# Kernel optimization log

Measured on AMD Instinct MI355X. Metric: run time of the kernel, lower is better.

## Reference

```python
import jax, jax.numpy as jnp
import numpy as np
from jax import lax

# --- hyperparameters from init_kwargs ---
THRESH = 0.5
TAU_M = 20.0
DT = 1.0
LENS = 0.5
GRAD_MAX = 1.0
DECAY = float(np.exp(-DT / TAU_M))  # leaky membrane decay (exp LUT approximated exactly)


@jax.custom_vjp
def spike_fn(v):
    # hard threshold spike
    return (v > THRESH).astype(v.dtype)


def _spike_fwd(v):
    return spike_fn(v), v


def _spike_bwd(v, g):
    # rectangular surrogate gradient (LUT-quantized in original; analytic here),
    # clipped at grad_max
    surr = jnp.minimum((jnp.abs(v - THRESH) < LENS).astype(g.dtype) / (2.0 * LENS), GRAD_MAX)
    return (g * surr,)


spike_fn.defvjp(_spike_fwd, _spike_bwd)


def conv2d(x, w):
    # NCHW, OIHW, stride 1, pad 1 (same)
    return lax.conv_general_dilated(x, w, (1, 1), [(1, 1), (1, 1)],
                                    dimension_numbers=('NCHW', 'OIHW', 'NCHW'))


def maxpool2(x):
    return lax.reduce_window(x, -jnp.inf, lax.max, (1, 1, 2, 2), (1, 1, 2, 2), 'VALID')


def lif_update(vm, s_prev, I):
    # leaky integrate with reset-by-subtraction via (1 - spike) gating
    vm = vm * DECAY * (1.0 - s_prev) + I
    return vm, spike_fn(vm)


def _xavier(key, shape, fan_in, fan_out):
    a = np.sqrt(6.0 / (fan_in + fan_out))
    return jax.random.uniform(key, shape, jnp.float32, -a, a)


def setup_inputs() -> dict:
    key = jax.random.key(0)
    k0, k1, k2, k3, k4 = jax.random.split(key, 5)
    B, T, C, H, W = 16, 16, 2, 64, 64
    inp = jax.random.uniform(k0, (B, T, C, H, W), jnp.float32)
    W0 = _xavier(k1, (32, 2, 3, 3), 2 * 9, 32 * 9)
    W1 = _xavier(k2, (64, 32, 3, 3), 32 * 9, 64 * 9)
    D0 = _xavier(k3, (512, 65536), 65536, 512)
    D1 = _xavier(k4, (11, 512), 512, 11)
    return {"input": inp, "W0": W0, "W1": W1, "D0": D0, "D1": D1,
            "batch_size": 16, "num_steps": 16, "limit": 1}


def reference(input, W0, W1, D0, D1, batch_size, num_steps, limit):
    B = batch_size
    vm0 = jnp.zeros((B, 32, 64, 64), jnp.float32); s0 = jnp.zeros_like(vm0)
    vm1 = jnp.zeros((B, 64, 64, 64), jnp.float32); s1 = jnp.zeros_like(vm1)
    vm2 = jnp.zeros((B, 512), jnp.float32); s2 = jnp.zeros_like(vm2)
    vm3 = jnp.zeros((B, 11), jnp.float32); s3 = jnp.zeros_like(vm3)
    acc = jnp.zeros((B, 11), jnp.float32)

    xs = jnp.swapaxes(input, 0, 1)  # [T, B, C, H, W] time-major for scan

    def step(carry, x_t):
        vm0, s0, vm1, s1, vm2, s2, vm3, s3, acc = carry
        in_spike = jnp.clip(x_t, 0.0, 1.0) if limit else x_t
        # conv layer 0 (no pool after layer 0 per original control flow)
        vm0, s0 = lif_update(vm0, s0, conv2d(in_spike, W0))
        # conv layer 1 (last conv): pool then flatten
        vm1, s1 = lif_update(vm1, s1, conv2d(s0, W1))
        flat = maxpool2(s1).reshape(s1.shape[0], -1)  # [B, 64*32*32]
        # dense layers
        vm2, s2 = lif_update(vm2, s2, flat @ D0.T)
        vm3, s3 = lif_update(vm3, s3, s2 @ D1.T)
        acc = acc + s3
        return (vm0, s0, vm1, s1, vm2, s2, vm3, s3, acc), None

    carry = (vm0, s0, vm1, s1, vm2, s2, vm3, s3, acc)
    carry, _ = lax.scan(step, carry, xs[:num_steps])
    return carry[-1] / num_steps
```

## Files before the change

### kernel.cpp

```cpp
#include <hip/hip_runtime.h>
#include <hip/hip_bf16.h>
#include <stdint.h>

#define DECAY 0.951229424500714f

#define BATCH 16
#define TSTEPS 16

#define OFF_S0BITS 0u
#define OFF_W0TB 4460544u
#define OFF_W1TB 4462848u
#define ZERO_BYTES 4460544u
#define KSPLIT 64
#define KCHUNK (65536 / KSPLIT)
#define OFF_PART_BYTES 0u
#define OFF_I_BYTES 33554432u
#define OFF_FLAT_BYTES 34078720u

typedef __attribute__((ext_vector_type(8))) short short8;
typedef __attribute__((ext_vector_type(4))) float floatx4;

__device__ inline unsigned short f2bf_rne(float f) {
    unsigned u = __float_as_uint(f);
    unsigned r = (u + 0x7FFFu + ((u >> 16) & 1u)) >> 16;
    return (unsigned short)r;
}
__device__ inline float bf2f(unsigned short h) {
    return __uint_as_float(((unsigned)h) << 16);
}

__global__ __launch_bounds__(256) void prep_weights(const float* __restrict__ W0,
                                                    const float* __restrict__ W1,
                                                    float* __restrict__ ws) {
    int id = blockIdx.x * 256 + threadIdx.x;
    if (id < 18432) {
        int oh = id / 9216, rem = id % 9216;
        int ic = rem / 288, rem2 = rem % 288;
        int k = rem2 / 32, ocl = rem2 % 32;
        int oc = oh * 32 + ocl;
        float* w1t = (float*)((char*)ws + OFF_W1TB);
        w1t[id] = W1[((size_t)oc * 32 + ic) * 9 + k];
    } else if (id < 19008) {
        int e = id - 18432;
        int ict = e >> 5, oc = e & 31;
        int ic = ict / 9, tap = ict % 9;
        float* w0t = (float*)((char*)ws + OFF_W0TB);
        w0t[ict * 32 + oc] = W0[(oc * 2 + ic) * 9 + tap];
    }
}

__global__ __launch_bounds__(256) void conv0_all(const float* __restrict__ in,
                                                 float* __restrict__ ws) {
    int b = blockIdx.x, y = blockIdx.y;
    int tid = threadIdx.x;
    int x = tid & 63;
    int g = __builtin_amdgcn_readfirstlane(tid >> 6);
    const float* w0t = (const float*)((const char*)ws + OFF_W0TB);
    unsigned char* s0b = (unsigned char*)((char*)ws + OFF_S0BITS);

    float vm[8];
#pragma unroll
    for (int u = 0; u < 8; ++u) vm[u] = 0.f;

    for (int t = 0; t < TSTEPS; ++t) {
        const float* xin = in + (size_t)((b * TSTEPS + t) * 2) * 4096;
        float acc[8];
#pragma unroll
        for (int u = 0; u < 8; ++u) acc[u] = 0.f;
#pragma unroll
        for (int ic = 0; ic < 2; ++ic) {
#pragma unroll
            for (int dy = 0; dy < 3; ++dy) {
                int sy = y + dy - 1;
                bool vy = (unsigned)sy < 64u;
                const float* rp = xin + ic * 4096 + sy * 64;
#pragma unroll
                for (int dx = 0; dx < 3; ++dx) {
                    int sx = x + dx - 1;
                    float v = (vy && (unsigned)sx < 64u) ? rp[sx] : 0.f;
                    v = fminf(fmaxf(v, 0.f), 1.f);
                    const float* wp = w0t + ((ic * 9 + dy * 3 + dx) * 32 + g * 8);
#pragma unroll
                    for (int u = 0; u < 8; ++u) acc[u] = fmaf(v, wp[u], acc[u]);
                }
            }
        }
        unsigned byte = 0;
#pragma unroll
        for (int u = 0; u < 8; ++u) {
            float v = ((vm[u] > 0.5f) ? 0.f : vm[u] * DECAY) + acc[u];
            vm[u] = v;
            if (v > 0.5f) byte |= (1u << u);
        }
        s0b[((size_t)(t * 16 + b) * 4356 + (size_t)(y + 1) * 66 + (x + 1)) * 4 + g] =
            (unsigned char)byte;
    }
}

__global__ __launch_bounds__(256, 4) void conv1_all(float* __restrict__ ws) {
    __shared__ float wlds[32 * 9 * 32];
    int tid = threadIdx.x;
    int j = tid & 31;
    int o4 = tid >> 5;
    int b = blockIdx.x, y2 = blockIdx.y, oh = blockIdx.z;
    int y0 = y2 * 2;

    {
        const float* wsrc = (const float*)((const char*)ws + OFF_W1TB) + (size_t)oh * 9216;
#pragma unroll
        for (int i = 0; i < 9; ++i) {
            int e = tid + i * 256;
            *(float4*)&wlds[e * 4] = *(const float4*)&wsrc[e * 4];
        }
    }
    __syncthreads();

    const unsigned* s0w = (const unsigned*)((const char*)ws + OFF_S0BITS);
    unsigned short* flat2 = (unsigned short*)((char*)ws + OFF_FLAT_BYTES);

    float vm1r[4][2][2];
#pragma unroll
    for (int u = 0; u < 4; ++u)
#pragma unroll
        for (int r = 0; r < 2; ++r)
#pragma unroll
            for (int c = 0; c < 2; ++c) vm1r[u][r][c] = 0.f;

    for (int t = 0; t < TSTEPS; ++t) {
        unsigned bits[4][4];
        {
            const unsigned* p = s0w + (size_t)(t * 16 + b) * 4356 + (size_t)y0 * 66 + 2 * j;
#pragma unroll
            for (int rr = 0; rr < 4; ++rr)
#pragma unroll
                for (int cc = 0; cc < 4; ++cc)
                    bits[rr][cc] = p[rr * 66 + cc];
        }
        unsigned orall = 0;
#pragma unroll
        for (int rr = 0; rr < 4; ++rr)
#pragma unroll
            for (int cc = 0; cc < 4; ++cc) orall |= bits[rr][cc];

        float acc[4][2][2];
#pragma unroll
        for (int u = 0; u < 4; ++u)
#pragma unroll
            for (int r = 0; r < 2; ++r)
#pragma unroll
                for (int c = 0; c < 2; ++c) acc[u][r][c] = 0.f;

        for (int ic = 0; ic < 32; ++ic) {
            if (__ballot((orall >> ic) & 1u) == 0ull) continue;
            float va[4][4];
#pragma unroll
            for (int rr = 0; rr < 4; ++rr)
#pragma unroll
                for (int cc = 0; cc < 4; ++cc)
                    va[rr][cc] = (float)((bits[rr][cc] >> ic) & 1u);
            const float* wic = &wlds[ic * 288 + o4 * 4];
#pragma unroll
            for (int k = 0; k < 9; ++k) {
                int kr = k / 3, kc = k - kr * 3;
                float4 wv = *(const float4*)&wic[k * 32];
                float wk[4] = {wv.x, wv.y, wv.z, wv.w};
#pragma unroll
                for (int u = 0; u < 4; ++u) {
                    float w = wk[u];
#pragma unroll
                    for (int r = 0; r < 2; ++r)
#pragma unroll
                        for (int c = 0; c < 2; ++c)
                            acc[u][r][c] = fmaf(va[kr + r][kc + c], w, acc[u][r][c]);
                }
            }
        }

        int m = t * 16 + b;
#pragma unroll
        for (int u = 0; u < 4; ++u) {
            int oc = oh * 32 + o4 * 4 + u;
            unsigned short por = 0;
#pragma unroll
            for (int r = 0; r < 2; ++r)
#pragma unroll
                for (int c = 0; c < 2; ++c) {
                    float v = vm1r[u][r][c];
                    v = ((v > 0.5f) ? 0.f : v * DECAY) + acc[u][r][c];
                    vm1r[u][r][c] = v;
                    if (v > 0.5f) por = 0x3F80;
                }
            int kg = oc * 128 + y2 * 4 + (j >> 3);
            flat2[((size_t)kg * 256 + m) * 8 + (j & 7)] = por;
        }
    }
}

__global__ __launch_bounds__(256) void dense0_mfma(const float* __restrict__ D0,
                                                   float* __restrict__ ws) {
    __shared__ unsigned short Bh_s[32 * 72];
    __shared__ unsigned short Bl_s[32 * 72];
    int tid = threadIdx.x;
    int kc = blockIdx.x, nb = blockIdx.y;
    int lane = tid & 63, w = tid >> 6, q = lane >> 4, r = lane & 15;
    const unsigned short* flat2 = (const unsigned short*)((const char*)ws + OFF_FLAT_BYTES);

    floatx4 acc[4][2];
#pragma unroll
    for (int i = 0; i < 4; ++i)
#pragma unroll
        for (int jj = 0; jj < 2; ++jj) acc[i][jj] = (floatx4){0.f, 0.f, 0.f, 0.f};

    int bn = tid & 31, bk8 = tid >> 5;
    const float* bG = D0 + (size_t)(nb * 32 + bn) * 65536 + (size_t)kc * KCHUNK + bk8 * 8;

    for (int k0 = 0; k0 < KCHUNK; k0 += 64) {
        short8 af[2][4];
#pragma unroll
        for (int ksi = 0; ksi < 2; ++ksi) {
            int kg = kc * 128 + (k0 >> 3) + ksi * 4 + q;
#pragma unroll
            for (int mi = 0; mi < 4; ++mi)
                af[ksi][mi] = *(const short8*)&flat2[((size_t)kg * 256
                                                     + (w * 64 + mi * 16 + r)) * 8];
        }
        float4 bv0 = *(const float4*)(bG + k0);
        float4 bv1 = *(const float4*)(bG + k0 + 4);

        __syncthreads();
        {
            float f[8] = {bv0.x, bv0.y, bv0.z, bv0.w, bv1.x, bv1.y, bv1.z, bv1.w};
            unsigned hw[4], lw[4];
#pragma unroll
            for (int jj = 0; jj < 4; ++jj) {
                unsigned short h0 = f2bf_rne(f[2*jj]),   h1 = f2bf_rne(f[2*jj+1]);
                unsigned short l0 = f2bf_rne(f[2*jj]   - bf2f(h0));
                unsigned short l1 = f2bf_rne(f[2*jj+1] - bf2f(h1));
                hw[jj] = (unsigned)h0 | ((unsigned)h1 << 16);
                lw[jj] = (unsigned)l0 | ((unsigned)l1 << 16);
            }
            *(uint4*)&Bh_s[bn * 72 + bk8 * 8] = make_uint4(hw[0], hw[1], hw[2], hw[3]);
            *(uint4*)&Bl_s[bn * 72 + bk8 * 8] = make_uint4(lw[0], lw[1], lw[2], lw[3]);
        }
        __syncthreads();

#pragma unroll
        for (int ksi = 0; ksi < 2; ++ksi) {
#pragma unroll
            for (int ni = 0; ni < 2; ++ni) {
                short8 bh = *(const short8*)&Bh_s[(ni * 16 + r) * 72 + ksi * 32 + q * 8];
                short8 bl = *(const short8*)&Bl_s[(ni * 16 + r) * 72 + ksi * 32 + q * 8];
#pragma unroll
                for (int mi = 0; mi < 4; ++mi) {
                    acc[mi][ni] = __builtin_amdgcn_mfma_f32_16x16x32_bf16(af[ksi][mi], bh, acc[mi][ni], 0, 0, 0);
                    acc[mi][ni] = __builtin_amdgcn_mfma_f32_16x16x32_bf16(af[ksi][mi], bl, acc[mi][ni], 0, 0, 0);
                }
            }
        }
    }

    float* part = (float*)((char*)ws + OFF_PART_BYTES);
#pragma unroll
    for (int mi = 0; mi < 4; ++mi)
#pragma unroll
        for (int ni = 0; ni < 2; ++ni) {
            int m0 = w * 64 + mi * 16 + q * 4;
            int n  = nb * 32 + ni * 16 + r;
#pragma unroll
            for (int rg = 0; rg < 4; ++rg)
                part[((size_t)kc * 256 + m0 + rg) * 512 + n] = acc[mi][ni][rg];
        }
}

__global__ __launch_bounds__(256) void reduce_part(float* __restrict__ ws) {
    int e = blockIdx.x * 256 + threadIdx.x;
    const float* part = (const float*)((const char*)ws + OFF_PART_BYTES);
    float s = 0.f;
#pragma unroll 8
    for (int c = 0; c < KSPLIT; ++c) s += part[(size_t)c * 131072 + e];
    ((float*)((char*)ws + OFF_I_BYTES))[e] = s;
}

__global__ __launch_bounds__(512) void tail_kernel(const float* __restrict__ D1,
                                                   float* __restrict__ out,
                                                   const float* __restrict__ ws_ro) {
    __shared__ float s2l[512];
    __shared__ float d1l[11 * 512];
    __shared__ float pb[2][11];
    int b = blockIdx.x;
    int tid = threadIdx.x;
    for (int i = tid; i < 11 * 512; i += 512) d1l[i] = D1[i];
    const float* Ibuf = (const float*)((const char*)ws_ro + OFF_I_BYTES);

    float vm2 = 0.f;
    unsigned s2 = 0u;
    float vm3 = 0.f, s3 = 0.f, accv = 0.f;
    __syncthreads();

    for (int t = 0; t < TSTEPS; ++t) {
        {
            float I = Ibuf[(size_t)(t * 16 + b) * 512 + tid];
            float sp = s2 ? 1.f : 0.f;
            float vm = vm2 * DECAY * (1.f - sp) + I;
            vm2 = vm;
            s2 = (vm > 0.5f) ? 1u : 0u;
            s2l[tid] = (float)s2;
        }
        __syncthreads();
        if (tid < 22) {
            int g = tid / 11, o = tid % 11;
            float p = 0.f;
            int kbase = g * 256;
            for (int k = 0; k < 256; ++k)
                p = fmaf(s2l[kbase + k], d1l[o * 512 + kbase + k], p);
            pb[g][o] = p;
        }
        __syncthreads();
        if (tid < 11) {
            float I3 = pb[0][tid] + pb[1][tid];
            float vm = vm3 * DECAY * (1.f - s3) + I3;
            vm3 = vm;
            s3 = (vm > 0.5f) ? 1.f : 0.f;
            accv += s3;
        }
        __syncthreads();
    }
    if (tid < 11) out[b * 11 + tid] = accv * (1.f / 16.f);
}

extern "C" void kernel_launch(void* const* d_in, const int* in_sizes, int n_in,
                              void* d_out, int out_size, void* d_ws, size_t ws_size,
                              hipStream_t stream) {
    (void)in_sizes; (void)n_in; (void)out_size; (void)ws_size;
    const float* in = (const float*)d_in[0];
    const float* W0 = (const float*)d_in[1];
    const float* W1 = (const float*)d_in[2];
    const float* D0 = (const float*)d_in[3];
    const float* D1 = (const float*)d_in[4];
    float* ws = (float*)d_ws;
    float* out = (float*)d_out;

    hipMemsetAsync(d_ws, 0, ZERO_BYTES, stream);
    prep_weights<<<75, 256, 0, stream>>>(W0, W1, ws);

    conv0_all<<<dim3(16, 64), 256, 0, stream>>>(in, ws);
    conv1_all<<<dim3(16, 32, 2), 256, 0, stream>>>(ws);

    dense0_mfma<<<dim3(KSPLIT, 16), 256, 0, stream>>>(D0, ws);
    reduce_part<<<512, 256, 0, stream>>>(ws);
    tail_kernel<<<16, 512, 0, stream>>>(D1, out, ws);
}
```

Before: 697.0 us.

## Double-buffer dense0 LDS tiles and prefetch next K-slice into registers

The dense0 MFMA kernel now keeps two LDS buffers for the bf16 hi/lo split of D0. It issues the global loads for the next 64-wide K slice, covering both the flat activations and D0, before running the MFMAs on the current slice, then converts and writes the next tile after compute. This cuts the loop to one barrier per iteration and is meant to hide global load latency behind MFMA work. In exchange it doubles LDS use and raises register pressure through the extra prefetch registers.

```diff
diff --git a/kernel.cpp b/kernel.cpp
--- a/kernel.cpp
+++ b/kernel.cpp
@@ -198,8 +198,8 @@
 
 __global__ __launch_bounds__(256) void dense0_mfma(const float* __restrict__ D0,
                                                    float* __restrict__ ws) {
-    __shared__ unsigned short Bh_s[32 * 72];
-    __shared__ unsigned short Bl_s[32 * 72];
+    __shared__ unsigned short Bh_s[2][32 * 72];
+    __shared__ unsigned short Bl_s[2][32 * 72];
     int tid = threadIdx.x;
     int kc = blockIdx.x, nb = blockIdx.y;
     int lane = tid & 63, w = tid >> 6, q = lane >> 4, r = lane & 15;
@@ -214,50 +214,76 @@
     int bn = tid & 31, bk8 = tid >> 5;
     const float* bG = D0 + (size_t)(nb * 32 + bn) * 65536 + (size_t)kc * KCHUNK + bk8 * 8;
 
-    for (int k0 = 0; k0 < KCHUNK; k0 += 64) {
-        short8 af[2][4];
+    auto convWrite = [&](int buf, float4 A, float4 B) {
+        float f[8] = {A.x, A.y, A.z, A.w, B.x, B.y, B.z, B.w};
+        unsigned hw[4], lw[4];
+#pragma unroll
+        for (int jj = 0; jj < 4; ++jj) {
+            unsigned short h0 = f2bf_rne(f[2*jj]),   h1 = f2bf_rne(f[2*jj+1]);
+            unsigned short l0 = f2bf_rne(f[2*jj]   - bf2f(h0));
+            unsigned short l1 = f2bf_rne(f[2*jj+1] - bf2f(h1));
+            hw[jj] = (unsigned)h0 | ((unsigned)h1 << 16);
+            lw[jj] = (unsigned)l0 | ((unsigned)l1 << 16);
+        }
+        *(uint4*)&Bh_s[buf][bn * 72 + bk8 * 8] = make_uint4(hw[0], hw[1], hw[2], hw[3]);
+        *(uint4*)&Bl_s[buf][bn * 72 + bk8 * 8] = make_uint4(lw[0], lw[1], lw[2], lw[3]);
+    };
+
+#define LOADA(dst, k0) do {                                                       \
+        _Pragma("unroll")                                                         \
+        for (int ksi_ = 0; ksi_ < 2; ++ksi_) {                                    \
+            int kg_ = kc * 128 + ((k0) >> 3) + ksi_ * 4 + q;                      \
+            _Pragma("unroll")                                                     \
+            for (int mi_ = 0; mi_ < 4; ++mi_)                                     \
+                dst[ksi_][mi_] = *(const short8*)&flat2[((size_t)kg_ * 256        \
+                                              + (w * 64 + mi_ * 16 + r)) * 8];    \
+        }                                                                         \
+    } while (0)
+
+    short8 afc[2][4], afn[2][4];
+    float4 bv0n, bv1n;
+
+    LOADA(afc, 0);
+    {
+        float4 b0 = *(const float4*)(bG);
+        float4 b1 = *(const float4*)(bG + 4);
+        convWrite(0, b0, b1);
+    }
+
+    for (int it = 0; it < 16; ++it) {
+        int cur = it & 1;
+        if (it < 15) {
+            int k0n = (it + 1) * 64;
+            LOADA(afn, k0n);
+            bv0n = *(const float4*)(bG + k0n);
+            bv1n = *(const float4*)(bG + k0n + 4);
+        }
+        __syncthreads();
+
 #pragma unroll
         for (int ksi = 0; ksi < 2; ++ksi) {
-            int kg = kc * 128 + (k0 >> 3) + ksi * 4 + q;
-#pragma unroll
-            for (int mi = 0; mi < 4; ++mi)
-                af[ksi][mi] = *(const short8*)&flat2[((size_t)kg * 256
-                                                     + (w * 64 + mi * 16 + r)) * 8];
-        }
-        float4 bv0 = *(const float4*)(bG + k0);
-        float4 bv1 = *(const float4*)(bG + k0 + 4);
-
-        __syncthreads();
-        {
-            float f[8] = {bv0.x, bv0.y, bv0.z, bv0.w, bv1.x, bv1.y, bv1.z, bv1.w};
-            unsigned hw[4], lw[4];
-#pragma unroll
-            for (int jj = 0; jj < 4; ++jj) {
-                unsigned short h0 = f2bf_rne(f[2*jj]),   h1 = f2bf_rne(f[2*jj+1]);
-                unsigned short l0 = f2bf_rne(f[2*jj]   - bf2f(h0));
-                unsigned short l1 = f2bf_rne(f[2*jj+1] - bf2f(h1));
-                hw[jj] = (unsigned)h0 | ((unsigned)h1 << 16);
-                lw[jj] = (unsigned)l0 | ((unsigned)l1 << 16);
-            }
-            *(uint4*)&Bh_s[bn * 72 + bk8 * 8] = make_uint4(hw[0], hw[1], hw[2], hw[3]);
-            *(uint4*)&Bl_s[bn * 72 + bk8 * 8] = make_uint4(lw[0], lw[1], lw[2], lw[3]);
-        }
-        __syncthreads();
-
-#pragma unroll
-        for (int ksi = 0; ksi < 2; ++ksi) {
 #pragma unroll
             for (int ni = 0; ni < 2; ++ni) {
-                short8 bh = *(const short8*)&Bh_s[(ni * 16 + r) * 72 + ksi * 32 + q * 8];
-                short8 bl = *(const short8*)&Bl_s[(ni * 16 + r) * 72 + ksi * 32 + q * 8];
+                short8 bh = *(const short8*)&Bh_s[cur][(ni * 16 + r) * 72 + ksi * 32 + q * 8];
+                short8 bl = *(const short8*)&Bl_s[cur][(ni * 16 + r) * 72 + ksi * 32 + q * 8];
 #pragma unroll
                 for (int mi = 0; mi < 4; ++mi) {
-                    acc[mi][ni] = __builtin_amdgcn_mfma_f32_16x16x32_bf16(af[ksi][mi], bh, acc[mi][ni], 0, 0, 0);
-                    acc[mi][ni] = __builtin_amdgcn_mfma_f32_16x16x32_bf16(af[ksi][mi], bl, acc[mi][ni], 0, 0, 0);
+                    acc[mi][ni] = __builtin_amdgcn_mfma_f32_16x16x32_bf16(afc[ksi][mi], bh, acc[mi][ni], 0, 0, 0);
+                    acc[mi][ni] = __builtin_amdgcn_mfma_f32_16x16x32_bf16(afc[ksi][mi], bl, acc[mi][ni], 0, 0, 0);
                 }
             }
         }
-    }
+
+        if (it < 15) {
+            convWrite(cur ^ 1, bv0n, bv1n);
+#pragma unroll
+            for (int ksi = 0; ksi < 2; ++ksi)
+#pragma unroll
+                for (int mi = 0; mi < 4; ++mi)
+                    afc[ksi][mi] = afn[ksi][mi];
+        }
+    }
+#undef LOADA
 
     float* part = (float*)((char*)ws + OFF_PART_BYTES);
 #pragma unroll
```

Result: no change. 687.0 us (-1.4%).
